# Performance work log

Hardware: AMD Instinct MI355X
Metric: run time of the kernel (lower is better)

The kernel has to match this reference:

```python
import jax, jax.numpy as jnp
import numpy as np

SEQ_LEN = 1024
BATCH = 256
HIDDEN = 100
OUT = 1

L_FILTER = [-0.0106, 0.0329, 0.0308, -0.187, -0.028, 0.6309, 0.7148, 0.2304]
H_FILTER = [-0.2304, 0.7148, -0.6309, -0.028, 0.187, 0.0308, -0.0329, -0.0106]


def _create_W(P, is_l, rng):
    filt = L_FILTER if is_l else H_FILTER
    eps = np.min(np.abs(filt))
    W = rng.standard_normal((P, P)) * 0.1 * eps
    for i in range(P):
        for k, j in enumerate(range(i, min(i + len(filt), P))):
            W[i, j] = filt[k]
    return jnp.asarray(W, dtype=jnp.float32)


def setup_inputs() -> dict:
    key = jax.random.key(0)
    ks = jax.random.split(key, 16)
    rng = np.random.default_rng(0)
    T, H = SEQ_LEN, HIDDEN
    s = 1.0 / np.sqrt(H)

    def lstm_params(k):
        k1, k2, k3 = jax.random.split(k, 3)
        Wih = jax.random.uniform(k1, (4 * H, 1), jnp.float32, -s, s)
        Whh = jax.random.uniform(k2, (4 * H, H), jnp.float32, -s, s)
        b = jax.random.uniform(k3, (4 * H,), jnp.float32, -s, s)
        return Wih, Whh, b

    Wih1, Whh1, b1 = lstm_params(ks[0])
    Wih2, Whh2, b2 = lstm_params(ks[1])
    Wih3, Whh3, b3 = lstm_params(ks[2])
    return {
        "x": jax.random.normal(ks[3], (BATCH, T, 1), jnp.float32),
        "W1H": _create_W(T, False, rng),
        "b1H": jax.random.uniform(ks[4], (T,), jnp.float32, -1 / np.sqrt(T), 1 / np.sqrt(T)),
        "W1L": _create_W(T, True, rng),
        "b1L": jax.random.uniform(ks[5], (T,), jnp.float32, -1 / np.sqrt(T), 1 / np.sqrt(T)),
        "W2H": _create_W(T // 2, False, rng),
        "b2H": jax.random.uniform(ks[6], (T // 2,), jnp.float32, -1 / np.sqrt(T // 2), 1 / np.sqrt(T // 2)),
        "W2L": _create_W(T // 2, True, rng),
        "b2L": jax.random.uniform(ks[7], (T // 2,), jnp.float32, -1 / np.sqrt(T // 2), 1 / np.sqrt(T // 2)),
        "Wih1": Wih1, "Whh1": Whh1, "b1": b1,
        "Wih2": Wih2, "Whh2": Whh2, "b2": b2,
        "Wih3": Wih3, "Whh3": Whh3, "b3": b3,
        "Wout": jax.random.uniform(ks[8], (OUT, H), jnp.float32, -s, s),
        "bout": jax.random.uniform(ks[9], (OUT,), jnp.float32, -s, s),
    }


def _avgpool2(x):  # [B, L] -> [B, L//2], AvgPool1d(kernel=2, stride=2)
    B, L = x.shape
    return x.reshape(B, L // 2, 2).mean(-1)


def _lstm(x, Wih, Whh, b):
    # x: [B, T, 1]; torch LSTM gate order i, f, g, o; h0 = c0 = 0
    H = Whh.shape[1]
    gx = jnp.einsum('bti,gi->btg', x, Wih) + b  # [B, T, 4H]

    def step(carry, g):
        h, c = carry
        z = g + h @ Whh.T
        i, f, gg, o = jnp.split(z, 4, axis=-1)
        c = jax.nn.sigmoid(f) * c + jax.nn.sigmoid(i) * jnp.tanh(gg)
        h = jax.nn.sigmoid(o) * jnp.tanh(c)
        return (h, c), h

    B = x.shape[0]
    h0 = jnp.zeros((B, H), x.dtype)
    _, hs = jax.lax.scan(step, (h0, h0), jnp.swapaxes(gx, 0, 1))
    return jnp.swapaxes(hs, 0, 1)  # [B, T, H]


def reference(x, W1H, b1H, W1L, b1L, W2H, b2H, W2L, b2L,
              Wih1, Whh1, b1, Wih2, Whh2, b2, Wih3, Whh3, b3, Wout, bout):
    inp = x[:, :, -1]  # [B, T]
    ah1 = jax.nn.sigmoid(inp @ W1H.T + b1H)
    al1 = jax.nn.sigmoid(inp @ W1L.T + b1L)
    xh1 = _avgpool2(ah1)  # [B, T/2]
    xl1 = _avgpool2(al1)  # [B, T/2]
    ah2 = jax.nn.sigmoid(xl1 @ W2H.T + b2H)
    al2 = jax.nn.sigmoid(xl1 @ W2L.T + b2L)
    xh2 = _avgpool2(ah2)  # [B, T/4]
    xl2 = _avgpool2(al2)  # [B, T/4]
    s1 = _lstm(xh1[..., None], Wih1, Whh1, b1)
    s2 = _lstm(xh2[..., None], Wih2, Whh2, b2)
    s3 = _lstm(xl2[..., None], Wih3, Whh3, b3)
    cat = jnp.concatenate([s1, s2, s3], axis=1)  # [B, T, H]
    out = cat @ Wout.T + bout  # [B, T, OUT]
    return out[:, -1, :]
```

## Files before the change

### kernel.cpp

```cpp
#include <hip/hip_runtime.h>
#include <math.h>

typedef __bf16 bf16x8 __attribute__((ext_vector_type(8)));
typedef _Float16 f16x8 __attribute__((ext_vector_type(8)));
typedef _Float16 f16x4 __attribute__((ext_vector_type(4)));
typedef float f32x4 __attribute__((ext_vector_type(4)));

__device__ __forceinline__ unsigned short f2bf(float f) {
  unsigned int u = __builtin_bit_cast(unsigned int, f);
  u += 0x7fffu + ((u >> 16) & 1u);
  return (unsigned short)(u >> 16);
}
__device__ __forceinline__ unsigned int pack2bf(float a, float b) {
  return (unsigned int)f2bf(a) | ((unsigned int)f2bf(b) << 16);
}

#define GK_PADK 40
template <int WFP32, int XFP32>
__global__ __launch_bounds__(256) void gemm_mfma_sig_pool(
    const void* __restrict__ Wv, const float* __restrict__ bias,
    const void* __restrict__ Xv, void* __restrict__ Y,
    int K, int Np, int out_bf16) {
  __shared__ unsigned short Wt[64][GK_PADK];
  __shared__ unsigned short Xt[64][GK_PADK];
  const int tid = threadIdx.x;
  const int i_base = blockIdx.x * 64;
  const int b_base = blockIdx.y * 64;
  const int srow = tid >> 2, sseg = tid & 3;
  const int wv = tid >> 6, lane = tid & 63;
  const int wn = wv & 1, wb = wv >> 1;
  const int L15 = lane & 15, q = lane >> 4;

  f32x4 acc[2][2] = {};
  for (int k0 = 0; k0 < K; k0 += 32) {
    if (WFP32) {
      const float* Wf = (const float*)Wv;
      const float4 a = *(const float4*)&Wf[(size_t)(i_base + srow) * K + k0 + sseg * 8];
      const float4 b = *(const float4*)&Wf[(size_t)(i_base + srow) * K + k0 + sseg * 8 + 4];
      uint4 p = { pack2bf(a.x, a.y), pack2bf(a.z, a.w), pack2bf(b.x, b.y), pack2bf(b.z, b.w) };
      *(uint4*)&Wt[srow][sseg * 8] = p;
    } else {
      *(uint4*)&Wt[srow][sseg * 8] =
          *(const uint4*)&((const unsigned short*)Wv)[(size_t)(i_base + srow) * K + k0 + sseg * 8];
    }
    if (XFP32) {
      const float* Xf = (const float*)Xv;
      const float4 a = *(const float4*)&Xf[(size_t)(b_base + srow) * K + k0 + sseg * 8];
      const float4 b = *(const float4*)&Xf[(size_t)(b_base + srow) * K + k0 + sseg * 8 + 4];
      uint4 p = { pack2bf(a.x, a.y), pack2bf(a.z, a.w), pack2bf(b.x, b.y), pack2bf(b.z, b.w) };
      *(uint4*)&Xt[srow][sseg * 8] = p;
    } else {
      *(uint4*)&Xt[srow][sseg * 8] =
          *(const uint4*)&((const unsigned short*)Xv)[(size_t)(b_base + srow) * K + k0 + sseg * 8];
    }
    __syncthreads();
    bf16x8 a0 = *(const bf16x8*)&Wt[wn * 32 + L15][q * 8];
    bf16x8 a1 = *(const bf16x8*)&Wt[wn * 32 + 16 + L15][q * 8];
    bf16x8 b0 = *(const bf16x8*)&Xt[wb * 32 + L15][q * 8];
    bf16x8 b1 = *(const bf16x8*)&Xt[wb * 32 + 16 + L15][q * 8];
    acc[0][0] = __builtin_amdgcn_mfma_f32_16x16x32_bf16(a0, b0, acc[0][0], 0, 0, 0);
    acc[0][1] = __builtin_amdgcn_mfma_f32_16x16x32_bf16(a0, b1, acc[0][1], 0, 0, 0);
    acc[1][0] = __builtin_amdgcn_mfma_f32_16x16x32_bf16(a1, b0, acc[1][0], 0, 0, 0);
    acc[1][1] = __builtin_amdgcn_mfma_f32_16x16x32_bf16(a1, b1, acc[1][1], 0, 0, 0);
    __syncthreads();
  }

  const int nb0 = i_base + wn * 32;
  const int bc0 = b_base + wb * 32 + L15;
#pragma unroll
  for (int mg = 0; mg < 2; mg++) {
    const int nrow = nb0 + mg * 16 + q * 4;
    const float bi0 = bias[nrow], bi1 = bias[nrow + 1];
    const float bi2 = bias[nrow + 2], bi3 = bias[nrow + 3];
#pragma unroll
    for (int bg = 0; bg < 2; bg++) {
      const int b = bc0 + bg * 16;
      f32x4 A = acc[mg][bg];
      const float a0 = __builtin_amdgcn_rcpf(1.f + __expf(-(A[0] + bi0)));
      const float a1 = __builtin_amdgcn_rcpf(1.f + __expf(-(A[1] + bi1)));
      const float a2 = __builtin_amdgcn_rcpf(1.f + __expf(-(A[2] + bi2)));
      const float a3 = __builtin_amdgcn_rcpf(1.f + __expf(-(A[3] + bi3)));
      const float p0 = 0.5f * (a0 + a1), p1 = 0.5f * (a2 + a3);
      const int pidx = nrow >> 1;
      if (out_bf16) {
        *(unsigned int*)&((unsigned short*)Y)[(size_t)b * Np + pidx] = pack2bf(p0, p1);
      } else {
        *(float2*)&((float*)Y)[(size_t)b * Np + pidx] = make_float2(p0, p1);
      }
    }
  }
}

__global__ __launch_bounds__(256) void prep_whh(
    const float* __restrict__ Whh, const float* __restrict__ b3,
    _Float16* __restrict__ P) {
  const int idx = blockIdx.x * 256 + threadIdx.x;
  if (idx >= 400 * 16) return;
  const int row = idx >> 4, ch = idx & 15;
  const int hid = row >> 2, gate = row & 3;
  const int src = gate * 100 + hid;
  f16x8 v;
#pragma unroll
  for (int j = 0; j < 8; j++) {
    const int k = ch * 8 + j;
    float f = 0.f;
    if (k < 100) f = Whh[(size_t)src * 100 + k];
    v[j] = (_Float16)f;
  }
  *(f16x8*)&P[(size_t)row * 128 + ch * 8] = v;
}

#define TSTEPS 256

__device__ __forceinline__ float qb0(float x) {
  return __builtin_bit_cast(float, __builtin_amdgcn_mov_dpp(__builtin_bit_cast(int, x), 0x00, 0xf, 0xf, true));
}
__device__ __forceinline__ float qb1(float x) {
  return __builtin_bit_cast(float, __builtin_amdgcn_mov_dpp(__builtin_bit_cast(int, x), 0x55, 0xf, 0xf, true));
}
__device__ __forceinline__ float qb2(float x) {
  return __builtin_bit_cast(float, __builtin_amdgcn_mov_dpp(__builtin_bit_cast(int, x), 0xAA, 0xf, 0xf, true));
}
__device__ __forceinline__ float qb3(float x) {
  return __builtin_bit_cast(float, __builtin_amdgcn_mov_dpp(__builtin_bit_cast(int, x), 0xFF, 0xf, 0xf, true));
}

__global__ __launch_bounds__(512, 2) void lstm_mfma(
    const float* __restrict__ X, const _Float16* __restrict__ P,
    const float* __restrict__ Whh, const float* __restrict__ Wih,
    const float* __restrict__ b3, const float* __restrict__ Wout,
    const float* __restrict__ bout, float* __restrict__ out) {
  const int bat = blockIdx.x;
  const int t = threadIdx.x;
  const int w = t >> 6, lane = t & 63;
  const int quad = lane >> 4, c = lane & 15;
  const int TB = (w == 7) ? 21 : w * 3;
  const int NT = (w == 7) ? 4 : 3;

  __shared__ __align__(16) _Float16 hbuf[2][128];
  __shared__ float xrow[TSTEPS];
  __shared__ float red[128];

  for (int i = t; i < TSTEPS; i += 512) xrow[i] = X[(size_t)bat * TSTEPS + i];
  if (t < 128) { hbuf[0][t] = (_Float16)0.f; hbuf[1][t] = (_Float16)0.f; }

#define LDA(J, KT) const f16x8 A##J##KT = \
    *(const f16x8*)&P[(size_t)((TB + J) * 16 + c) * 128 + (KT) * 32 + quad * 8];
  LDA(0,0) LDA(0,1) LDA(0,2)
  LDA(1,0) LDA(1,1) LDA(1,2)
  LDA(2,0) LDA(2,1) LDA(2,2)
  LDA(3,0) LDA(3,1) LDA(3,2)
#undef LDA

  const bool act = (c < 4 * NT);
  const int J = c >> 2, g = c & 3;
  const int myhid = 4 * (TB + (act ? J : 0)) + quad;
  const int grow = g * 100 + myhid;
  const float u_ = Wih[grow];
  const float bz = b3[grow];
  const float4 wt = *(const float4*)&Whh[(size_t)grow * 100 + 96];
  const float kk = (g == 2) ? 2.f : 1.f;
  const float mm = (g == 2) ? 2.f : 1.f;
  const float dd = (g == 2) ? -1.f : 0.f;
  float cst = 0.f;
  __syncthreads();

#define SIG(zz) __builtin_amdgcn_rcpf(1.f + __expf(-(zz)))
#define STEPB(HC, HN, XT)                                                      \
  {                                                                            \
    const _Float16* hc = (HC);                                                 \
    const f16x8 B0 = *(const f16x8*)&hc[0 * 32 + quad * 8];                    \
    const f16x8 B1 = *(const f16x8*)&hc[1 * 32 + quad * 8];                    \
    const f16x8 B2 = *(const f16x8*)&hc[2 * 32 + quad * 8];                    \
    f32x4 z0 = {0.f,0.f,0.f,0.f}, z1 = z0, z2 = z0, z3 = z0;                   \
    { f32x4 za = z0, zb = z0;                                                  \
      za = __builtin_amdgcn_mfma_f32_16x16x32_f16(A00, B0, za, 0, 0, 0);       \
      zb = __builtin_amdgcn_mfma_f32_16x16x32_f16(A01, B1, zb, 0, 0, 0);       \
      za = __builtin_amdgcn_mfma_f32_16x16x32_f16(A02, B2, za, 0, 0, 0);       \
      z0 = za + zb; }                                                          \
    { f32x4 za = {0.f,0.f,0.f,0.f}, zb = za;                                   \
      za = __builtin_amdgcn_mfma_f32_16x16x32_f16(A10, B0, za, 0, 0, 0);       \
      zb = __builtin_amdgcn_mfma_f32_16x16x32_f16(A11, B1, zb, 0, 0, 0);       \
      za = __builtin_amdgcn_mfma_f32_16x16x32_f16(A12, B2, za, 0, 0, 0);       \
      z1 = za + zb; }                                                          \
    { f32x4 za = {0.f,0.f,0.f,0.f}, zb = za;                                   \
      za = __builtin_amdgcn_mfma_f32_16x16x32_f16(A20, B0, za, 0, 0, 0);       \
      zb = __builtin_amdgcn_mfma_f32_16x16x32_f16(A21, B1, zb, 0, 0, 0);       \
      za = __builtin_amdgcn_mfma_f32_16x16x32_f16(A22, B2, za, 0, 0, 0);       \
      z2 = za + zb; }                                                          \
    if (w == 7) {                                                              \
      f32x4 za = {0.f,0.f,0.f,0.f}, zb = za;                                   \
      za = __builtin_amdgcn_mfma_f32_16x16x32_f16(A30, B0, za, 0, 0, 0);       \
      zb = __builtin_amdgcn_mfma_f32_16x16x32_f16(A31, B1, zb, 0, 0, 0);       \
      za = __builtin_amdgcn_mfma_f32_16x16x32_f16(A32, B2, za, 0, 0, 0);       \
      z3 = za + zb; }                                                          \
    if (act) {                                                                 \
      const f32x4 zt = (J == 0) ? z0 : (J == 1) ? z1 : (J == 2) ? z2 : z3;     \
      float zs = (g == 0) ? zt[0] : (g == 1) ? zt[1] : (g == 2) ? zt[2] : zt[3];\
      const f16x4 ht = *(const f16x4*)&hc[96];                                 \
      zs = fmaf(wt.x, (float)ht[0], zs);                                       \
      zs = fmaf(wt.y, (float)ht[1], zs);                                       \
      zs = fmaf(wt.z, (float)ht[2], zs);                                       \
      zs = fmaf(wt.w, (float)ht[3], zs);                                       \
      zs = fmaf(u_, (XT), zs + bz);                                            \
      const float a = mm * SIG(kk * zs) + dd;                                  \
      const float ai = qb0(a), af = qb1(a), ag = qb2(a), ao = qb3(a);          \
      cst = fmaf(af, cst, ai * ag);                                            \
      const float th = 2.f * SIG(2.f * cst) - 1.f;                             \
      if (g == 0) (HN)[myhid] = (_Float16)(ao * th);                           \
    }                                                                          \
    __syncthreads();                                                           \
  }

  for (int step = 0; step < TSTEPS; step += 2) {
    STEPB(hbuf[0], hbuf[1], xrow[step]);
    STEPB(hbuf[1], hbuf[0], xrow[step + 1]);
  }
#undef STEPB
#undef SIG

  if (t < 128) {
    float a = 0.f;
    if (t < 100) a = (float)hbuf[0][t] * Wout[t];
    red[t] = a;
  }
  __syncthreads();
  if (t == 0) {
    float s = 0.f;
#pragma unroll
    for (int k = 0; k < 128; k++) s += red[k];
    out[bat] = s + bout[0];
  }
}

extern "C" void kernel_launch(void* const* d_in, const int* in_sizes, int n_in,
                              void* d_out, int out_size, void* d_ws, size_t ws_size,
                              hipStream_t stream) {
  const float* x    = (const float*)d_in[0];
  const float* W1L  = (const float*)d_in[3];
  const float* b1L  = (const float*)d_in[4];
  const float* W2L  = (const float*)d_in[7];
  const float* b2L  = (const float*)d_in[8];
  const float* Wih3 = (const float*)d_in[15];
  const float* Whh3 = (const float*)d_in[16];
  const float* b3   = (const float*)d_in[17];
  const float* Wout = (const float*)d_in[18];
  const float* bout = (const float*)d_in[19];
  float* out = (float*)d_out;

  unsigned short* xl1b = (unsigned short*)d_ws;
  float* xl2 = (float*)(xl1b + (size_t)256 * 512);
  _Float16* P = (_Float16*)(xl2 + (size_t)256 * 256);

  prep_whh<<<25, 256, 0, stream>>>(Whh3, b3, P);
  gemm_mfma_sig_pool<1, 1><<<dim3(16, 4), 256, 0, stream>>>(W1L, b1L, x, xl1b, 1024, 512, 1);
  gemm_mfma_sig_pool<1, 0><<<dim3(8, 4), 256, 0, stream>>>(W2L, b2L, xl1b, xl2, 512, 256, 0);
  lstm_mfma<<<256, 512, 0, stream>>>(xl2, P, Whh3, Wih3, b3, Wout, bout, out);
}
```

Baseline: 262.8 us.

## Batch 16 sequences per LSTM block using the MFMA N dimension

The recurrent LSTM kernel now processes 16 batch elements per block, using the 16 MFMA columns for separate sequences instead of one sequence per block. Launch size drops from 256 blocks to 16. Each lane now receives all four gates of a hidden unit directly from the MFMA output, which removes the DPP cross-lane shuffles. The padded K=128 MFMA replaces the scalar tail over hidden units 96–99, and the bias is folded into the accumulator init. The hidden state moves to a swizzled [16][128] f16 shared buffer to avoid bank conflicts. In exchange, each lane does about four times more transcendental work per step, and only 16 CUs are active, so per-step serial latency may rise.

After: 345.7 us. +31.6%, slower.

```diff
diff --git a/kernel.cpp b/kernel.cpp
--- a/kernel.cpp
+++ b/kernel.cpp
@@ -111,127 +111,128 @@
 }
 
 #define TSTEPS 256
-
-__device__ __forceinline__ float qb0(float x) {
-  return __builtin_bit_cast(float, __builtin_amdgcn_mov_dpp(__builtin_bit_cast(int, x), 0x00, 0xf, 0xf, true));
-}
-__device__ __forceinline__ float qb1(float x) {
-  return __builtin_bit_cast(float, __builtin_amdgcn_mov_dpp(__builtin_bit_cast(int, x), 0x55, 0xf, 0xf, true));
-}
-__device__ __forceinline__ float qb2(float x) {
-  return __builtin_bit_cast(float, __builtin_amdgcn_mov_dpp(__builtin_bit_cast(int, x), 0xAA, 0xf, 0xf, true));
-}
-__device__ __forceinline__ float qb3(float x) {
-  return __builtin_bit_cast(float, __builtin_amdgcn_mov_dpp(__builtin_bit_cast(int, x), 0xFF, 0xf, 0xf, true));
-}
-
-__global__ __launch_bounds__(512, 2) void lstm_mfma(
+#define SIG(zz) __builtin_amdgcn_rcpf(1.f + __expf(-(zz)))
+
+__global__ __launch_bounds__(512, 2) void lstm_mfma16(
     const float* __restrict__ X, const _Float16* __restrict__ P,
-    const float* __restrict__ Whh, const float* __restrict__ Wih,
-    const float* __restrict__ b3, const float* __restrict__ Wout,
-    const float* __restrict__ bout, float* __restrict__ out) {
-  const int bat = blockIdx.x;
+    const float* __restrict__ Wih, const float* __restrict__ b3,
+    const float* __restrict__ Wout, const float* __restrict__ bout,
+    float* __restrict__ out) {
+  const int b0 = blockIdx.x * 16;
   const int t = threadIdx.x;
   const int w = t >> 6, lane = t & 63;
   const int quad = lane >> 4, c = lane & 15;
   const int TB = (w == 7) ? 21 : w * 3;
   const int NT = (w == 7) ? 4 : 3;
 
-  __shared__ __align__(16) _Float16 hbuf[2][128];
-  __shared__ float xrow[TSTEPS];
-  __shared__ float red[128];
-
-  for (int i = t; i < TSTEPS; i += 512) xrow[i] = X[(size_t)bat * TSTEPS + i];
-  if (t < 128) { hbuf[0][t] = (_Float16)0.f; hbuf[1][t] = (_Float16)0.f; }
-
-#define LDA(J, KT) const f16x8 A##J##KT = \
-    *(const f16x8*)&P[(size_t)((TB + J) * 16 + c) * 128 + (KT) * 32 + quad * 8];
-  LDA(0,0) LDA(0,1) LDA(0,2)
-  LDA(1,0) LDA(1,1) LDA(1,2)
-  LDA(2,0) LDA(2,1) LDA(2,2)
-  LDA(3,0) LDA(3,1) LDA(3,2)
-#undef LDA
-
-  const bool act = (c < 4 * NT);
-  const int J = c >> 2, g = c & 3;
-  const int myhid = 4 * (TB + (act ? J : 0)) + quad;
-  const int grow = g * 100 + myhid;
-  const float u_ = Wih[grow];
-  const float bz = b3[grow];
-  const float4 wt = *(const float4*)&Whh[(size_t)grow * 100 + 96];
-  const float kk = (g == 2) ? 2.f : 1.f;
-  const float mm = (g == 2) ? 2.f : 1.f;
-  const float dd = (g == 2) ? -1.f : 0.f;
-  float cst = 0.f;
+  __shared__ __align__(16) _Float16 hb[2][2048];
+  __shared__ float xq[TSTEPS * 16];
+  __shared__ float red[512];
+
+  for (int idx = t; idx < 16 * TSTEPS; idx += 512) {
+    const int bb = idx >> 8, s = idx & 255;
+    xq[s * 16 + bb] = X[(size_t)(b0 + bb) * TSTEPS + s];
+  }
+  {
+    const float4 z4 = {0.f, 0.f, 0.f, 0.f};
+    ((float4*)hb)[t] = z4;
+  }
+
+  f16x8 A[4][4];
+#pragma unroll
+  for (int J = 0; J < 4; J++)
+    if (J < NT) {
+#pragma unroll
+      for (int kt = 0; kt < 4; kt++)
+        A[J][kt] = *(const f16x8*)&P[(size_t)((TB + J) * 16 + c) * 128 + kt * 32 + quad * 8];
+    }
+
+  f32x4 b3p[4], wihp[4];
+#pragma unroll
+  for (int J = 0; J < 4; J++)
+    if (J < NT) {
+      const int hid = 4 * (TB + J) + quad;
+#pragma unroll
+      for (int r = 0; r < 4; r++) {
+        const int src = r * 100 + hid;
+        b3p[J][r] = b3[src];
+        wihp[J][r] = Wih[src];
+      }
+    }
+
+  const int swz = (c & 7) << 4;
+  int roff[4], woff[4];
+#pragma unroll
+  for (int kt = 0; kt < 4; kt++) roff[kt] = c * 256 + ((kt * 64 + quad * 16) ^ swz);
+#pragma unroll
+  for (int J = 0; J < 4; J++) woff[J] = c * 256 + ((8 * (TB + J) + 2 * quad) ^ swz);
+
+  float cst[4] = {0.f, 0.f, 0.f, 0.f};
   __syncthreads();
 
-#define SIG(zz) __builtin_amdgcn_rcpf(1.f + __expf(-(zz)))
-#define STEPB(HC, HN, XT)                                                      \
-  {                                                                            \
-    const _Float16* hc = (HC);                                                 \
-    const f16x8 B0 = *(const f16x8*)&hc[0 * 32 + quad * 8];                    \
-    const f16x8 B1 = *(const f16x8*)&hc[1 * 32 + quad * 8];                    \
-    const f16x8 B2 = *(const f16x8*)&hc[2 * 32 + quad * 8];                    \
-    f32x4 z0 = {0.f,0.f,0.f,0.f}, z1 = z0, z2 = z0, z3 = z0;                   \
-    { f32x4 za = z0, zb = z0;                                                  \
-      za = __builtin_amdgcn_mfma_f32_16x16x32_f16(A00, B0, za, 0, 0, 0);       \
-      zb = __builtin_amdgcn_mfma_f32_16x16x32_f16(A01, B1, zb, 0, 0, 0);       \
-      za = __builtin_amdgcn_mfma_f32_16x16x32_f16(A02, B2, za, 0, 0, 0);       \
-      z0 = za + zb; }                                                          \
-    { f32x4 za = {0.f,0.f,0.f,0.f}, zb = za;                                   \
-      za = __builtin_amdgcn_mfma_f32_16x16x32_f16(A10, B0, za, 0, 0, 0);       \
-      zb = __builtin_amdgcn_mfma_f32_16x16x32_f16(A11, B1, zb, 0, 0, 0);       \
-      za = __builtin_amdgcn_mfma_f32_16x16x32_f16(A12, B2, za, 0, 0, 0);       \
-      z1 = za + zb; }                                                          \
-    { f32x4 za = {0.f,0.f,0.f,0.f}, zb = za;                                   \
-      za = __builtin_amdgcn_mfma_f32_16x16x32_f16(A20, B0, za, 0, 0, 0);       \
-      zb = __builtin_amdgcn_mfma_f32_16x16x32_f16(A21, B1, zb, 0, 0, 0);       \
-      za = __builtin_amdgcn_mfma_f32_16x16x32_f16(A22, B2, za, 0, 0, 0);       \
-      z2 = za + zb; }                                                          \
-    if (w == 7) {                                                              \
-      f32x4 za = {0.f,0.f,0.f,0.f}, zb = za;                                   \
-      za = __builtin_amdgcn_mfma_f32_16x16x32_f16(A30, B0, za, 0, 0, 0);       \
-      zb = __builtin_amdgcn_mfma_f32_16x16x32_f16(A31, B1, zb, 0, 0, 0);       \
-      za = __builtin_amdgcn_mfma_f32_16x16x32_f16(A32, B2, za, 0, 0, 0);       \
-      z3 = za + zb; }                                                          \
-    if (act) {                                                                 \
-      const f32x4 zt = (J == 0) ? z0 : (J == 1) ? z1 : (J == 2) ? z2 : z3;     \
-      float zs = (g == 0) ? zt[0] : (g == 1) ? zt[1] : (g == 2) ? zt[2] : zt[3];\
-      const f16x4 ht = *(const f16x4*)&hc[96];                                 \
-      zs = fmaf(wt.x, (float)ht[0], zs);                                       \
-      zs = fmaf(wt.y, (float)ht[1], zs);                                       \
-      zs = fmaf(wt.z, (float)ht[2], zs);                                       \
-      zs = fmaf(wt.w, (float)ht[3], zs);                                       \
-      zs = fmaf(u_, (XT), zs + bz);                                            \
-      const float a = mm * SIG(kk * zs) + dd;                                  \
-      const float ai = qb0(a), af = qb1(a), ag = qb2(a), ao = qb3(a);          \
-      cst = fmaf(af, cst, ai * ag);                                            \
-      const float th = 2.f * SIG(2.f * cst) - 1.f;                             \
-      if (g == 0) (HN)[myhid] = (_Float16)(ao * th);                           \
-    }                                                                          \
-    __syncthreads();                                                           \
-  }
-
-  for (int step = 0; step < TSTEPS; step += 2) {
-    STEPB(hbuf[0], hbuf[1], xrow[step]);
-    STEPB(hbuf[1], hbuf[0], xrow[step + 1]);
-  }
-#undef STEPB
+#define STEP(CUR, NXT, XV)                                                    \
+  {                                                                           \
+    const char* hcb = (const char*)hb[CUR];                                   \
+    char* hnb = (char*)hb[NXT];                                               \
+    const f16x8 B0 = *(const f16x8*)(hcb + roff[0]);                          \
+    const f16x8 B1 = *(const f16x8*)(hcb + roff[1]);                          \
+    const f16x8 B2 = *(const f16x8*)(hcb + roff[2]);                          \
+    const f16x8 B3 = *(const f16x8*)(hcb + roff[3]);                          \
+    _Pragma("unroll")                                                         \
+    for (int J = 0; J < 4; J++)                                               \
+      if (J < NT) {                                                           \
+        f32x4 z = b3p[J];                                                     \
+        z = __builtin_amdgcn_mfma_f32_16x16x32_f16(A[J][0], B0, z, 0, 0, 0);  \
+        z = __builtin_amdgcn_mfma_f32_16x16x32_f16(A[J][1], B1, z, 0, 0, 0);  \
+        z = __builtin_amdgcn_mfma_f32_16x16x32_f16(A[J][2], B2, z, 0, 0, 0);  \
+        z = __builtin_amdgcn_mfma_f32_16x16x32_f16(A[J][3], B3, z, 0, 0, 0);  \
+        const float zi = fmaf(wihp[J][0], (XV), z[0]);                        \
+        const float zf = fmaf(wihp[J][1], (XV), z[1]);                        \
+        const float zg = fmaf(wihp[J][2], (XV), z[2]);                        \
+        const float zo = fmaf(wihp[J][3], (XV), z[3]);                        \
+        const float ai = SIG(zi);                                             \
+        const float af = SIG(zf);                                             \
+        const float ag = 2.f * SIG(2.f * zg) - 1.f;                           \
+        const float ao = SIG(zo);                                             \
+        cst[J] = fmaf(af, cst[J], ai * ag);                                   \
+        const float th = 2.f * SIG(2.f * cst[J]) - 1.f;                       \
+        *(_Float16*)(hnb + woff[J]) = (_Float16)(ao * th);                    \
+      }                                                                       \
+    __syncthreads();                                                         \
+  }
+
+  for (int s = 0; s < TSTEPS; s += 2) {
+    const float xv0 = xq[s * 16 + c];
+    const float xv1 = xq[s * 16 + 16 + c];
+    STEP(0, 1, xv0);
+    STEP(1, 0, xv1);
+  }
+#undef STEP
+
+  {
+    const int cc = t >> 5, j = t & 31;
+    const char* hfb = (const char*)hb[0];
+    const int sw = (cc & 7) << 4;
+    float acc = 0.f;
+#pragma unroll
+    for (int m = 0; m < 4; m++) {
+      const int hid = j + 32 * m;
+      if (hid < 100) {
+        const _Float16 hv = *(const _Float16*)(hfb + cc * 256 + ((2 * hid) ^ sw));
+        acc += (float)hv * Wout[hid];
+      }
+    }
+    red[t] = acc;
+  }
+  __syncthreads();
+  if (t < 16) {
+    float s = 0.f;
+#pragma unroll
+    for (int k = 0; k < 32; k++) s += red[t * 32 + k];
+    out[b0 + t] = s + bout[0];
+  }
+}
 #undef SIG
-
-  if (t < 128) {
-    float a = 0.f;
-    if (t < 100) a = (float)hbuf[0][t] * Wout[t];
-    red[t] = a;
-  }
-  __syncthreads();
-  if (t == 0) {
-    float s = 0.f;
-#pragma unroll
-    for (int k = 0; k < 128; k++) s += red[k];
-    out[bat] = s + bout[0];
-  }
-}
 
 extern "C" void kernel_launch(void* const* d_in, const int* in_sizes, int n_in,
                               void* d_out, int out_size, void* d_ws, size_t ws_size,
@@ -255,5 +256,5 @@
   prep_whh<<<25, 256, 0, stream>>>(Whh3, b3, P);
   gemm_mfma_sig_pool<1, 1><<<dim3(16, 4), 256, 0, stream>>>(W1L, b1L, x, xl1b, 1024, 512, 1);
   gemm_mfma_sig_pool<1, 0><<<dim3(8, 4), 256, 0, stream>>>(W2L, b2L, xl1b, xl2, 512, 256, 0);
-  lstm_mfma<<<256, 512, 0, stream>>>(xl2, P, Whh3, Wih3, b3, Wout, bout, out);
-}
+  lstm_mfma16<<<16, 512, 0, stream>>>(xl2, P, Wih3, b3, Wout, bout, out);
+}
```

## Double-buffer GEMM K loop with register prefetch; prescale LSTM weights for exp2

Applied to the files above, without the earlier changes.

The filter GEMM kernel now processes 64-wide K tiles and prefetches the next tile's global loads into registers before staging the current tile to LDS. This halves the barrier count per K and overlaps load latency with the MFMA work. Separately, the LSTM weights, bias and input weights are prescaled by log2(e) (twice that for the tanh gate) so the sigmoids can use a raw exp2 instead of __expf, which removes a multiply from the serial step. Prescaling the fp16 recurrent weights slightly changes their rounding, and the extra prefetch registers raise register pressure.

After: 241.6 us. 8.1% less time.

```diff
diff --git a/kernel.cpp b/kernel.cpp
--- a/kernel.cpp
+++ b/kernel.cpp
@@ -15,14 +15,14 @@
   return (unsigned int)f2bf(a) | ((unsigned int)f2bf(b) << 16);
 }
 
-#define GK_PADK 40
+#define GK_PAD2 72
 template <int WFP32, int XFP32>
 __global__ __launch_bounds__(256) void gemm_mfma_sig_pool(
     const void* __restrict__ Wv, const float* __restrict__ bias,
     const void* __restrict__ Xv, void* __restrict__ Y,
     int K, int Np, int out_bf16) {
-  __shared__ unsigned short Wt[64][GK_PADK];
-  __shared__ unsigned short Xt[64][GK_PADK];
+  __shared__ unsigned short Wt[64][GK_PAD2];
+  __shared__ unsigned short Xt[64][GK_PAD2];
   const int tid = threadIdx.x;
   const int i_base = blockIdx.x * 64;
   const int b_base = blockIdx.y * 64;
@@ -31,39 +31,118 @@
   const int wn = wv & 1, wb = wv >> 1;
   const int L15 = lane & 15, q = lane >> 4;
 
+  const float* Wf = (const float*)Wv;
+  const float* Xf = (const float*)Xv;
+  const unsigned short* Wh = (const unsigned short*)Wv;
+  const unsigned short* Xh = (const unsigned short*)Xv;
+
+  float4 wf[2][4], xf[2][4];
+  uint4 wh[2][2], xh[2][2];
+
+#define LOADW(S, KO)                                                          \
+  do {                                                                        \
+    if (WFP32) {                                                              \
+      _Pragma("unroll") for (int j = 0; j < 4; j++)                           \
+          wf[S][j] = *(const float4*)&Wf[(size_t)(i_base + srow) * K + (KO) + \
+                                         sseg * 16 + 4 * j];                  \
+    } else {                                                                  \
+      _Pragma("unroll") for (int j = 0; j < 2; j++)                           \
+          wh[S][j] = *(const uint4*)&Wh[(size_t)(i_base + srow) * K + (KO) +  \
+                                        sseg * 16 + 8 * j];                   \
+    }                                                                         \
+  } while (0)
+
+#define LOADX(S, KO)                                                          \
+  do {                                                                        \
+    if (XFP32) {                                                              \
+      _Pragma("unroll") for (int j = 0; j < 4; j++)                           \
+          xf[S][j] = *(const float4*)&Xf[(size_t)(b_base + srow) * K + (KO) + \
+                                         sseg * 16 + 4 * j];                  \
+    } else {                                                                  \
+      _Pragma("unroll") for (int j = 0; j < 2; j++)                           \
+          xh[S][j] = *(const uint4*)&Xh[(size_t)(b_base + srow) * K + (KO) +  \
+                                        sseg * 16 + 8 * j];                   \
+    }                                                                         \
+  } while (0)
+
+#define STAGEW(S)                                                             \
+  do {                                                                        \
+    if (WFP32) {                                                              \
+      uint4 p0 = {pack2bf(wf[S][0].x, wf[S][0].y),                            \
+                  pack2bf(wf[S][0].z, wf[S][0].w),                            \
+                  pack2bf(wf[S][1].x, wf[S][1].y),                            \
+                  pack2bf(wf[S][1].z, wf[S][1].w)};                           \
+      uint4 p1 = {pack2bf(wf[S][2].x, wf[S][2].y),                            \
+                  pack2bf(wf[S][2].z, wf[S][2].w),                            \
+                  pack2bf(wf[S][3].x, wf[S][3].y),                            \
+                  pack2bf(wf[S][3].z, wf[S][3].w)};                           \
+      *(uint4*)&Wt[srow][sseg * 16] = p0;                                     \
+      *(uint4*)&Wt[srow][sseg * 16 + 8] = p1;                                 \
+    } else {                                                                  \
+      *(uint4*)&Wt[srow][sseg * 16] = wh[S][0];                               \
+      *(uint4*)&Wt[srow][sseg * 16 + 8] = wh[S][1];                           \
+    }                                                                         \
+  } while (0)
+
+#define STAGEX(S)                                                             \
+  do {                                                                        \
+    if (XFP32) {                                                              \
+      uint4 p0 = {pack2bf(xf[S][0].x, xf[S][0].y),                            \
+                  pack2bf(xf[S][0].z, xf[S][0].w),                            \
+                  pack2bf(xf[S][1].x, xf[S][1].y),                            \
+                  pack2bf(xf[S][1].z, xf[S][1].w)};                           \
+      uint4 p1 = {pack2bf(xf[S][2].x, xf[S][2].y),                            \
+                  pack2bf(xf[S][2].z, xf[S][2].w),                            \
+                  pack2bf(xf[S][3].x, xf[S][3].y),                            \
+                  pack2bf(xf[S][3].z, xf[S][3].w)};                           \
+      *(uint4*)&Xt[srow][sseg * 16] = p0;                                     \
+      *(uint4*)&Xt[srow][sseg * 16 + 8] = p1;                                 \
+    } else {                                                                  \
+      *(uint4*)&Xt[srow][sseg * 16] = xh[S][0];                               \
+      *(uint4*)&Xt[srow][sseg * 16 + 8] = xh[S][1];                           \
+    }                                                                         \
+  } while (0)
+
+#define DOMFMA                                                                \
+  do {                                                                        \
+    _Pragma("unroll") for (int kt = 0; kt < 2; kt++) {                        \
+      bf16x8 a0 = *(const bf16x8*)&Wt[wn * 32 + L15][kt * 32 + q * 8];        \
+      bf16x8 a1 = *(const bf16x8*)&Wt[wn * 32 + 16 + L15][kt * 32 + q * 8];   \
+      bf16x8 b0 = *(const bf16x8*)&Xt[wb * 32 + L15][kt * 32 + q * 8];        \
+      bf16x8 b1 = *(const bf16x8*)&Xt[wb * 32 + 16 + L15][kt * 32 + q * 8];   \
+      acc[0][0] = __builtin_amdgcn_mfma_f32_16x16x32_bf16(a0, b0, acc[0][0], 0, 0, 0); \
+      acc[0][1] = __builtin_amdgcn_mfma_f32_16x16x32_bf16(a0, b1, acc[0][1], 0, 0, 0); \
+      acc[1][0] = __builtin_amdgcn_mfma_f32_16x16x32_bf16(a1, b0, acc[1][0], 0, 0, 0); \
+      acc[1][1] = __builtin_amdgcn_mfma_f32_16x16x32_bf16(a1, b1, acc[1][1], 0, 0, 0); \
+    }                                                                         \
+  } while (0)
+
   f32x4 acc[2][2] = {};
-  for (int k0 = 0; k0 < K; k0 += 32) {
-    if (WFP32) {
-      const float* Wf = (const float*)Wv;
-      const float4 a = *(const float4*)&Wf[(size_t)(i_base + srow) * K + k0 + sseg * 8];
-      const float4 b = *(const float4*)&Wf[(size_t)(i_base + srow) * K + k0 + sseg * 8 + 4];
-      uint4 p = { pack2bf(a.x, a.y), pack2bf(a.z, a.w), pack2bf(b.x, b.y), pack2bf(b.z, b.w) };
-      *(uint4*)&Wt[srow][sseg * 8] = p;
-    } else {
-      *(uint4*)&Wt[srow][sseg * 8] =
-          *(const uint4*)&((const unsigned short*)Wv)[(size_t)(i_base + srow) * K + k0 + sseg * 8];
+  LOADW(0, 0);
+  LOADX(0, 0);
+  for (int k0 = 0; k0 < K; k0 += 128) {
+    LOADW(1, k0 + 64);
+    LOADX(1, k0 + 64);
+    STAGEW(0);
+    STAGEX(0);
+    __syncthreads();
+    DOMFMA;
+    __syncthreads();
+    if (k0 + 128 < K) {
+      LOADW(0, k0 + 128);
+      LOADX(0, k0 + 128);
     }
-    if (XFP32) {
-      const float* Xf = (const float*)Xv;
-      const float4 a = *(const float4*)&Xf[(size_t)(b_base + srow) * K + k0 + sseg * 8];
-      const float4 b = *(const float4*)&Xf[(size_t)(b_base + srow) * K + k0 + sseg * 8 + 4];
-      uint4 p = { pack2bf(a.x, a.y), pack2bf(a.z, a.w), pack2bf(b.x, b.y), pack2bf(b.z, b.w) };
-      *(uint4*)&Xt[srow][sseg * 8] = p;
-    } else {
-      *(uint4*)&Xt[srow][sseg * 8] =
-          *(const uint4*)&((const unsigned short*)Xv)[(size_t)(b_base + srow) * K + k0 + sseg * 8];
-    }
+    STAGEW(1);
+    STAGEX(1);
     __syncthreads();
-    bf16x8 a0 = *(const bf16x8*)&Wt[wn * 32 + L15][q * 8];
-    bf16x8 a1 = *(const bf16x8*)&Wt[wn * 32 + 16 + L15][q * 8];
-    bf16x8 b0 = *(const bf16x8*)&Xt[wb * 32 + L15][q * 8];
-    bf16x8 b1 = *(const bf16x8*)&Xt[wb * 32 + 16 + L15][q * 8];
-    acc[0][0] = __builtin_amdgcn_mfma_f32_16x16x32_bf16(a0, b0, acc[0][0], 0, 0, 0);
-    acc[0][1] = __builtin_amdgcn_mfma_f32_16x16x32_bf16(a0, b1, acc[0][1], 0, 0, 0);
-    acc[1][0] = __builtin_amdgcn_mfma_f32_16x16x32_bf16(a1, b0, acc[1][0], 0, 0, 0);
-    acc[1][1] = __builtin_amdgcn_mfma_f32_16x16x32_bf16(a1, b1, acc[1][1], 0, 0, 0);
+    DOMFMA;
     __syncthreads();
   }
+#undef LOADW
+#undef LOADX
+#undef STAGEW
+#undef STAGEX
+#undef DOMFMA
 
   const int nb0 = i_base + wn * 32;
   const int bc0 = b_base + wb * 32 + L15;
@@ -91,6 +170,8 @@
   }
 }
 
+#define LOG2E 1.44269504f
+#define TWOL2E 2.88539008f
 __global__ __launch_bounds__(256) void prep_whh(
     const float* __restrict__ Whh, const float* __restrict__ b3,
     _Float16* __restrict__ P) {
@@ -99,12 +180,13 @@
   const int row = idx >> 4, ch = idx & 15;
   const int hid = row >> 2, gate = row & 3;
   const int src = gate * 100 + hid;
+  const float s = (gate == 2) ? TWOL2E : LOG2E;
   f16x8 v;
 #pragma unroll
   for (int j = 0; j < 8; j++) {
     const int k = ch * 8 + j;
     float f = 0.f;
-    if (k < 100) f = Whh[(size_t)src * 100 + k];
+    if (k < 100) f = Whh[(size_t)src * 100 + k] * s;
     v[j] = (_Float16)f;
   }
   *(f16x8*)&P[(size_t)row * 128 + ch * 8] = v;
@@ -156,16 +238,17 @@
   const int J = c >> 2, g = c & 3;
   const int myhid = 4 * (TB + (act ? J : 0)) + quad;
   const int grow = g * 100 + myhid;
-  const float u_ = Wih[grow];
-  const float bz = b3[grow];
-  const float4 wt = *(const float4*)&Whh[(size_t)grow * 100 + 96];
-  const float kk = (g == 2) ? 2.f : 1.f;
+  const float sc = (g == 2) ? TWOL2E : LOG2E;
+  const float u_ = Wih[grow] * sc;
+  const float bz = b3[grow] * sc;
+  const float4 wt0 = *(const float4*)&Whh[(size_t)grow * 100 + 96];
+  const float4 wt = make_float4(wt0.x * sc, wt0.y * sc, wt0.z * sc, wt0.w * sc);
   const float mm = (g == 2) ? 2.f : 1.f;
   const float dd = (g == 2) ? -1.f : 0.f;
   float cst = 0.f;
   __syncthreads();
 
-#define SIG(zz) __builtin_amdgcn_rcpf(1.f + __expf(-(zz)))
+#define SIG2(zz) __builtin_amdgcn_rcpf(1.f + __builtin_amdgcn_exp2f(-(zz)))
 #define STEPB(HC, HN, XT)                                                      \
   {                                                                            \
     const _Float16* hc = (HC);                                                 \
@@ -203,10 +286,10 @@
       zs = fmaf(wt.z, (float)ht[2], zs);                                       \
       zs = fmaf(wt.w, (float)ht[3], zs);                                       \
       zs = fmaf(u_, (XT), zs + bz);                                            \
-      const float a = mm * SIG(kk * zs) + dd;                                  \
+      const float a = mm * SIG2(zs) + dd;                                      \
       const float ai = qb0(a), af = qb1(a), ag = qb2(a), ao = qb3(a);          \
       cst = fmaf(af, cst, ai * ag);                                            \
-      const float th = 2.f * SIG(2.f * cst) - 1.f;                             \
+      const float th = 2.f * SIG2(TWOL2E * cst) - 1.f;                         \
       if (g == 0) (HN)[myhid] = (_Float16)(ao * th);                           \
     }                                                                          \
     __syncthreads();                                                           \
@@ -217,7 +300,7 @@
     STEPB(hbuf[1], hbuf[0], xrow[step + 1]);
   }
 #undef STEPB
-#undef SIG
+#undef SIG2
 
   if (t < 128) {
     float a = 0.f;
```
